# Kernel optimization log

Measured on AMD Instinct MI355X. Metric: run time of the kernel, lower is better.

## Reference

```python
import jax, jax.numpy as jnp
import numpy as np

P = 4096        # n_particles
D = 64          # embedding_dim
H = 4           # attention heads
HD = D // H     # head dim
N = 1_000_000   # n_collisions


def setup_inputs() -> dict:
    key = jax.random.key(0)
    ks = jax.random.split(key, 24)
    s = lambda k, shape, fan: jax.random.normal(k, shape, jnp.float32) / np.sqrt(fan)
    inp = {
        'times': jax.random.normal(ks[0], (N,), jnp.float32),
        'momentum_transfers': jax.random.normal(ks[1], (N,), jnp.float32),
        'positions': jax.random.normal(ks[2], (N,), jnp.float32),
        'particle_pairs': jax.random.randint(ks[3], (N, 2), 0, P),
        # event encoder: Linear(3, D)
        'W_enc': s(ks[4], (3, D), 3), 'b_enc': jnp.zeros((D,), jnp.float32),
        # learned particle embeddings
        'pemb': s(ks[5], (P, D), D),
        # MultiheadAttention projections (math layout: y = x @ W + b)
        'Wq': s(ks[6], (D, D), D), 'bq': jnp.zeros((D,), jnp.float32),
        'Wk': s(ks[7], (D, D), D), 'bk': jnp.zeros((D,), jnp.float32),
        'Wv': s(ks[8], (D, D), D), 'bv': jnp.zeros((D,), jnp.float32),
        'Wo': s(ks[9], (D, D), D), 'bo': jnp.zeros((D,), jnp.float32),
        # mass head: Linear(D, D//2) -> ReLU -> Linear(D//2, 1) -> Softplus
        'Wm1': s(ks[10], (D, D // 2), D), 'bm1': jnp.zeros((D // 2,), jnp.float32),
        'Wm2': s(ks[11], (D // 2, 1), D // 2), 'bm2': jnp.zeros((1,), jnp.float32),
        # diameter head
        'Wd1': s(ks[12], (D, D // 2), D), 'bd1': jnp.zeros((D // 2,), jnp.float32),
        'Wd2': s(ks[13], (D // 2, 1), D // 2), 'bd2': jnp.zeros((1,), jnp.float32),
    }
    return inp


def _forward(times, momentum_transfers, positions, particle_pairs,
             W_enc, b_enc, pemb, Wq, bq, Wk, bk, Wv, bv, Wo, bo,
             Wm1, bm1, Wm2, bm2, Wd1, bd1, Wd2, bd2):
    # 1. embed collision events: (N,3) -> (N,D), tanh
    feats = jnp.stack([times, momentum_transfers, positions], axis=-1)
    emb = jnp.tanh(feats @ W_enc + b_enc)  # (N, D)

    # 2. segment-mean pooling into particle bins (both endpoints of each pair)
    idx = particle_pairs.reshape(-1)                     # (2N,)
    vals = jnp.repeat(emb, 2, axis=0)                    # (2N, D) [p1,p2 per event]
    updates = jax.ops.segment_sum(vals, idx, num_segments=P)          # (P, D)
    counts = jax.ops.segment_sum(jnp.ones_like(idx, jnp.float32), idx,
                                 num_segments=P)                      # (P,)
    counts = jnp.clip(counts, 1.0)
    x = pemb + updates / counts[:, None]                 # (P, D)

    # 3. self-attention over particles (batch of 1)
    q = (x @ Wq + bq).reshape(P, H, HD)
    k = (x @ Wk + bk).reshape(P, H, HD)
    v = (x @ Wv + bv).reshape(P, H, HD)
    scale = 1.0 / np.sqrt(HD)
    scores = jnp.einsum('phd,qhd->hpq', q * scale, k)    # (H, P, P)
    attn = jax.nn.softmax(scores, axis=-1)
    ctx = jnp.einsum('hpq,qhd->phd', attn, v).reshape(P, D)
    x = ctx @ Wo + bo                                    # (P, D)

    # 4. prediction heads
    masses = jax.nn.softplus(
        (jax.nn.relu(x @ Wm1 + bm1) @ Wm2 + bm2)).squeeze(-1)  # (P,)
    diameters = jax.nn.softplus(
        (jax.nn.relu(x @ Wd1 + bd1) @ Wd2 + bd2)).squeeze(-1)  # (P,)
    return masses, diameters


def reference(times, momentum_transfers, positions, particle_pairs,
              W_enc, b_enc, pemb, Wq, bq, Wk, bk, Wv, bv, Wo, bo,
              Wm1, bm1, Wm2, bm2, Wd1, bd1, Wd2, bd2):
    return _forward(times, momentum_transfers, positions, particle_pairs,
                    W_enc, b_enc, pemb, Wq, bq, Wk, bk, Wv, bv, Wo, bo,
                    Wm1, bm1, Wm2, bm2, Wd1, bd1, Wd2, bd2)
```

## Files before the change

### kernel.cpp

```cpp
#include <hip/hip_runtime.h>
#include <hip/hip_fp16.h>
#include <math.h>

#define NP 1000000
#define NE (2 * NP)
#define P 4096
#define D 64
#define H 4
#define HD 16

#define NB 512
#define PBT 1024
#define SCB 128

#define KC 8

typedef short s4v __attribute__((ext_vector_type(4)));
typedef short s8v __attribute__((ext_vector_type(8)));
typedef float f4v __attribute__((ext_vector_type(4)));

__device__ __forceinline__ float softplus_f(float x) {
    return fmaxf(x, 0.0f) + log1pf(__expf(-fabsf(x)));
}
__device__ __forceinline__ unsigned short f2bf_rne(float f) {
    unsigned int b = __float_as_uint(f);
    b += 0x7fffu + ((b >> 16) & 1u);
    return (unsigned short)(b >> 16);
}

__global__ void __launch_bounds__(PBT) hist_pass(const int* __restrict__ pairs,
                                                 int* __restrict__ hists) {
    __shared__ int lh[P];
    const int tid = threadIdx.x, blk = blockIdx.x;
    for (int i = tid; i < P; i += PBT) lh[i] = 0;
    __syncthreads();
    const int lo = (int)(((long long)blk * NE) / NB);
    const int hi = (int)(((long long)(blk + 1) * NE) / NB);
    for (int i = lo + tid; i < hi; i += PBT) atomicAdd(&lh[pairs[i]], 1);
    __syncthreads();
    for (int i = tid; i < P; i += PBT) hists[(size_t)blk * P + i] = lh[i];
}

__global__ void __launch_bounds__(1024) scan_cols(int* __restrict__ hists,
                                                  int* __restrict__ totals) {
    __shared__ int buf[64][SCB];
    const int bo = blockIdx.x * SCB;
    const int t = threadIdx.x;
    const int col = t & (SCB - 1);
    const int row = t >> 7;
    int carry = 0;
    for (int c = 0; c < NB / 64; ++c) {
#pragma unroll
        for (int r8 = 0; r8 < 64; r8 += 8)
            buf[r8 + row][col] = hists[(size_t)(c * 64 + r8 + row) * P + bo + col];
        __syncthreads();
        if (t < SCB) {
            int cr = carry;
            for (int r = 0; r < 64; ++r) { int v = buf[r][t]; buf[r][t] = cr; cr += v; }
            carry = cr;
        }
        __syncthreads();
#pragma unroll
        for (int r8 = 0; r8 < 64; r8 += 8)
            hists[(size_t)(c * 64 + r8 + row) * P + bo + col] = buf[r8 + row][col];
        __syncthreads();
    }
    if (t < SCB) totals[bo + t] = carry;
}

__global__ void __launch_bounds__(1024) scan_bins(const int* __restrict__ totals,
                                                  int* __restrict__ bin_start) {
    __shared__ int sdat[1024];
    const int t = threadIdx.x;
    int a[4]; int s = 0;
#pragma unroll
    for (int k2 = 0; k2 < 4; ++k2) { a[k2] = totals[t * 4 + k2]; s += a[k2]; }
    sdat[t] = s;
    __syncthreads();
    for (int off = 1; off < 1024; off <<= 1) {
        int v = (t >= off) ? sdat[t - off] : 0;
        __syncthreads();
        sdat[t] += v;
        __syncthreads();
    }
    int run = sdat[t] - s;
#pragma unroll
    for (int k2 = 0; k2 < 4; ++k2) { bin_start[t * 4 + k2] = run; run += a[k2]; }
    if (t == 1023) bin_start[P] = run;
}

__global__ void __launch_bounds__(PBT) place_pass(
        const int* __restrict__ pairs, const float* __restrict__ times,
        const float* __restrict__ mom, const float* __restrict__ pos,
        const int* __restrict__ hists, const int* __restrict__ bin_start,
        uint2* __restrict__ sfeats) {
    __shared__ int lc[P];
    __shared__ int loff[P];
    const int tid = threadIdx.x, blk = blockIdx.x;
    for (int i = tid; i < P; i += PBT) {
        lc[i] = 0;
        loff[i] = bin_start[i] + hists[(size_t)blk * P + i];
    }
    __syncthreads();
    const int lo = (int)(((long long)blk * NE) / NB);
    const int hi = (int)(((long long)(blk + 1) * NE) / NB);
    int idx[4]; bool vld[4]; int bb[4]; uint2 ff[4];
#pragma unroll
    for (int j = 0; j < 4; ++j) {
        idx[j] = lo + tid + j * PBT;
        vld[j] = idx[j] < hi;
        int i2 = vld[j] ? idx[j] : lo;
        int ev = i2 >> 1;
        bb[j] = pairs[i2];
        __half2 tm = __floats2half2_rn(times[ev], mom[ev]);
        __half2 pz = __floats2half2_rn(pos[ev], 0.0f);
        ff[j].x = *(unsigned int*)&tm;
        ff[j].y = *(unsigned int*)&pz;
    }
    int rr[4];
#pragma unroll
    for (int j = 0; j < 4; ++j)
        rr[j] = vld[j] ? atomicAdd(&lc[bb[j]], 1) : 0;
#pragma unroll
    for (int j = 0; j < 4; ++j)
        if (vld[j]) sfeats[(size_t)loff[bb[j]] + rr[j]] = ff[j];
}

#define PDIM(w0_, w1_, w2_, b_, j)                                             \
    {                                                                          \
        float uA = fmaf(fAx, w0_, fmaf(fAy, w1_, fmaf(fAz, w2_, b_)));         \
        float uB = fmaf(fBx, w0_, fmaf(fBy, w1_, fmaf(fBz, w2_, b_)));         \
        float pA = __builtin_amdgcn_exp2f(uA) + 1.0f;                          \
        float pB = __builtin_amdgcn_exp2f(uB) + 1.0f;                          \
        racc[j] = fmaf(pA + pB, __builtin_amdgcn_rcpf(pA * pB), racc[j]);      \
    }
#define GBODY2()                                                               \
    PDIM(w0a[0], w1a[0], w2a[0], ba[0], 0)                                     \
    PDIM(w0a[1], w1a[1], w2a[1], ba[1], 1)                                     \
    PDIM(w0a[2], w1a[2], w2a[2], ba[2], 2)                                     \
    PDIM(w0a[3], w1a[3], w2a[3], ba[3], 3)                                     \
    PDIM(w0b[0], w1b[0], w2b[0], bbv[0], 4)                                    \
    PDIM(w0b[1], w1b[1], w2b[1], bbv[1], 5)                                    \
    PDIM(w0b[2], w1b[2], w2b[2], bbv[2], 6)                                    \
    PDIM(w0b[3], w1b[3], w2b[3], bbv[3], 7)

#define SDIM(w0_, w1_, w2_, b_, j)                                             \
    {                                                                          \
        float u = fmaf(fAx, w0_, fmaf(fAy, w1_, fmaf(fAz, w2_, b_)));          \
        racc[j] += __builtin_amdgcn_rcpf(__builtin_amdgcn_exp2f(u) + 1.0f);    \
    }
#define GBODY1()                                                               \
    SDIM(w0a[0], w1a[0], w2a[0], ba[0], 0)                                     \
    SDIM(w0a[1], w1a[1], w2a[1], ba[1], 1)                                     \
    SDIM(w0a[2], w1a[2], w2a[2], ba[2], 2)                                     \
    SDIM(w0a[3], w1a[3], w2a[3], ba[3], 3)                                     \
    SDIM(w0b[0], w1b[0], w2b[0], bbv[0], 4)                                    \
    SDIM(w0b[1], w1b[1], w2b[1], bbv[1], 5)                                    \
    SDIM(w0b[2], w1b[2], w2b[2], bbv[2], 6)                                    \
    SDIM(w0b[3], w1b[3], w2b[3], bbv[3], 7)

__global__ void __launch_bounds__(512) gather_kernel(
        const uint2* __restrict__ sfeats, const int* __restrict__ bin_start,
        const float* __restrict__ Wenc, const float* __restrict__ benc,
        const float* __restrict__ pemb, float* __restrict__ x) {
    __shared__ float sred[2][32][68];
    const int tid = threadIdx.x;
    const int wv = tid >> 6, ln = tid & 63;
    const int bi = wv >> 2, qh = wv & 3;
    const int es = ln & 7, dg = ln >> 3;
    const int b = blockIdx.x * 2 + bi;
    const int d0 = dg * 8;
    const float C = 2.8853900817779268f;
    f4v w0a = *(const f4v*)(Wenc + d0);          f4v w0b = *(const f4v*)(Wenc + d0 + 4);
    f4v w1a = *(const f4v*)(Wenc + D + d0);      f4v w1b = *(const f4v*)(Wenc + D + d0 + 4);
    f4v w2a = *(const f4v*)(Wenc + 2 * D + d0);  f4v w2b = *(const f4v*)(Wenc + 2 * D + d0 + 4);
    f4v ba  = *(const f4v*)(benc + d0);          f4v bbv = *(const f4v*)(benc + d0 + 4);
    w0a *= C; w0b *= C; w1a *= C; w1b *= C; w2a *= C; w2b *= C; ba *= C; bbv *= C;

    const int s0 = bin_start[b], s1 = bin_start[b + 1];
    const int cnt = s1 - s0;
    const int qs = (cnt + 3) >> 2;
    const int lo = s0 + qh * qs;
    const int hi = min(s0 + (qh + 1) * qs, s1);

    float racc[8];
#pragma unroll
    for (int j = 0; j < 8; ++j) racc[j] = 0.0f;
    int ncnt = 0;
    int base = lo;
    for (; base + 16 <= hi; base += 16) {
        uint2 uA = sfeats[base + es];
        uint2 uB = sfeats[base + 8 + es];
        float2 tA = __half22float2(*(__half2*)&uA.x);
        float fAx = tA.x, fAy = tA.y, fAz = __half2float(*(__half*)&uA.y);
        float2 tB = __half22float2(*(__half2*)&uB.x);
        float fBx = tB.x, fBy = tB.y, fBz = __half2float(*(__half*)&uB.y);
        GBODY2();
        ncnt += 2;
    }
    if (base + 8 <= hi) {
        uint2 uA = sfeats[base + es];
        float2 tA = __half22float2(*(__half2*)&uA.x);
        float fAx = tA.x, fAy = tA.y, fAz = __half2float(*(__half*)&uA.y);
        GBODY1();
        ncnt += 1;
        base += 8;
    }
    if (base < hi) {
        const int n = hi - base;
        const bool valid = es < n;
        uint2 uA = valid ? sfeats[base + es] : make_uint2(0u, 0u);
        float2 tA = __half22float2(*(__half2*)&uA.x);
        float fAx = tA.x, fAy = tA.y, fAz = __half2float(*(__half*)&uA.y);
        float save[8];
#pragma unroll
        for (int j = 0; j < 8; ++j) save[j] = racc[j];
        GBODY1();
        if (!valid) {
#pragma unroll
            for (int j = 0; j < 8; ++j) racc[j] = save[j];
        } else {
            ncnt += 1;
        }
    }
    const float fn = (float)ncnt;
    float* sw = &sred[bi][qh * 8 + es][d0];
#pragma unroll
    for (int j = 0; j < 8; ++j) sw[j] = fmaf(-2.0f, racc[j], fn);
    __syncthreads();
    if (tid < 128) {
        int bin = tid >> 6, dim = tid & 63;
        float s = 0.0f;
#pragma unroll
        for (int e2 = 0; e2 < 32; ++e2) s += sred[bin][e2][dim];
        int gb = blockIdx.x * 2 + bin;
        float c2 = (float)(bin_start[gb + 1] - bin_start[gb]);
        x[gb * D + dim] = pemb[gb * D + dim] + s / fmaxf(c2, 1.0f);
    }
}

__global__ void qkv_kernel(const float* __restrict__ x,
                           const float* __restrict__ Wq, const float* __restrict__ bq,
                           const float* __restrict__ Wk, const float* __restrict__ bk,
                           const float* __restrict__ Wv, const float* __restrict__ bv,
                           unsigned short* __restrict__ Qb, unsigned short* __restrict__ Kf,
                           unsigned short* __restrict__ Vf) {
    __shared__ float xs[4][D];
    const int r0 = blockIdx.x * 4;
    const int tid = threadIdx.x;
    xs[tid >> 6][tid & 63] = x[r0 * D + tid];
    __syncthreads();
    const int row = tid >> 6, col = tid & 63;
    float aq = bq[col], ak = bk[col], av = bv[col];
    for (int d = 0; d < D; ++d) {
        float xv = xs[row][d];
        aq = fmaf(xv, Wq[d * D + col], aq);
        ak = fmaf(xv, Wk[d * D + col], ak);
        av = fmaf(xv, Wv[d * D + col], av);
    }
    const int h = col >> 4, hd = col & 15, gr = r0 + row;
    Qb[((h * P + gr) << 4) + hd] = f2bf_rne(aq * 0.3606737602222409f);
    const int kb = gr >> 5, kk = gr & 31, up = kk >> 4;
    Kf[(((size_t)h * 128 + kb) * 64 + (hd >> 2) * 16 + (kk & 15)) * 8 + up * 4 + (hd & 3)] =
        f2bf_rne(ak);
    Vf[(((size_t)h * 128 + kb) * 64 + ((kk & 15) >> 2) * 16 + hd) * 8 + up * 4 + (kk & 3)] =
        f2bf_rne(av);
}

__global__ void __launch_bounds__(256) flash_kernel(
        const unsigned short* __restrict__ Qb, const unsigned short* __restrict__ Kf,
        const unsigned short* __restrict__ Vf,
        float* __restrict__ pl, float* __restrict__ pout) {
    const int bid = blockIdx.x;
    const int h  = bid & 3;
    const int qt = (bid >> 2) & 63;
    const int kc = bid >> 8;
    const int tid = threadIdx.x;
    const int wv = tid >> 6, lane = tid & 63;
    const int g = lane >> 4, li = lane & 15;
    const int q0 = qt * 64 + wv * 16;

    s8v qf = {0, 0, 0, 0, 0, 0, 0, 0};
    {
        s4v ql = *(const s4v*)(Qb + ((size_t)(h * P + q0 + li) << 4) + 4 * g);
        qf[0] = ql[0]; qf[1] = ql[1]; qf[2] = ql[2]; qf[3] = ql[3];
    }
    const unsigned short* Kh = Kf + (size_t)h * 128 * 512;
    const unsigned short* Vh = Vf + (size_t)h * 128 * 512;

    f4v accA = {0.f, 0.f, 0.f, 0.f};
    f4v accB = {0.f, 0.f, 0.f, 0.f};
    float lA = 0.f, lB = 0.f;
    const int kb0 = kc * (P / KC / 32);
    const int kb1 = kb0 + P / KC / 32;
#pragma unroll 4
    for (int kb = kb0; kb < kb1; kb += 2) {
        s8v kf1 = *(const s8v*)(Kh + ((size_t)kb * 64 + lane) * 8);
        s8v kf2 = *(const s8v*)(Kh + ((size_t)(kb + 1) * 64 + lane) * 8);
        s8v vf1 = *(const s8v*)(Vh + ((size_t)kb * 64 + lane) * 8);
        s8v vf2 = *(const s8v*)(Vh + ((size_t)(kb + 1) * 64 + lane) * 8);
        s8v ka1 = {kf1[0], kf1[1], kf1[2], kf1[3], 0, 0, 0, 0};
        s8v ka2 = {kf1[4], kf1[5], kf1[6], kf1[7], 0, 0, 0, 0};
        s8v ka3 = {kf2[0], kf2[1], kf2[2], kf2[3], 0, 0, 0, 0};
        s8v ka4 = {kf2[4], kf2[5], kf2[6], kf2[7], 0, 0, 0, 0};
        f4v z = {0.f, 0.f, 0.f, 0.f};
        f4v c1 = __builtin_amdgcn_mfma_f32_16x16x32_bf16(ka1, qf, z, 0, 0, 0);
        f4v c2 = __builtin_amdgcn_mfma_f32_16x16x32_bf16(ka2, qf, z, 0, 0, 0);
        f4v c3 = __builtin_amdgcn_mfma_f32_16x16x32_bf16(ka3, qf, z, 0, 0, 0);
        f4v c4 = __builtin_amdgcn_mfma_f32_16x16x32_bf16(ka4, qf, z, 0, 0, 0);
        float p0 = __builtin_amdgcn_exp2f(c1[0]), p1 = __builtin_amdgcn_exp2f(c1[1]);
        float p2 = __builtin_amdgcn_exp2f(c1[2]), p3 = __builtin_amdgcn_exp2f(c1[3]);
        float p4 = __builtin_amdgcn_exp2f(c2[0]), p5 = __builtin_amdgcn_exp2f(c2[1]);
        float p6 = __builtin_amdgcn_exp2f(c2[2]), p7 = __builtin_amdgcn_exp2f(c2[3]);
        float p8 = __builtin_amdgcn_exp2f(c3[0]), p9 = __builtin_amdgcn_exp2f(c3[1]);
        float pa = __builtin_amdgcn_exp2f(c3[2]), pb = __builtin_amdgcn_exp2f(c3[3]);
        float pc = __builtin_amdgcn_exp2f(c4[0]), pd = __builtin_amdgcn_exp2f(c4[1]);
        float pe = __builtin_amdgcn_exp2f(c4[2]), pf_ = __builtin_amdgcn_exp2f(c4[3]);
        lA += ((p0 + p1) + (p2 + p3)) + ((p4 + p5) + (p6 + p7));
        lB += ((p8 + p9) + (pa + pb)) + ((pc + pd) + (pe + pf_));
        s8v pf1, pf2;
        pf1[0] = (short)(__float_as_uint(p0) >> 16); pf1[1] = (short)(__float_as_uint(p1) >> 16);
        pf1[2] = (short)(__float_as_uint(p2) >> 16); pf1[3] = (short)(__float_as_uint(p3) >> 16);
        pf1[4] = (short)(__float_as_uint(p4) >> 16); pf1[5] = (short)(__float_as_uint(p5) >> 16);
        pf1[6] = (short)(__float_as_uint(p6) >> 16); pf1[7] = (short)(__float_as_uint(p7) >> 16);
        pf2[0] = (short)(__float_as_uint(p8) >> 16); pf2[1] = (short)(__float_as_uint(p9) >> 16);
        pf2[2] = (short)(__float_as_uint(pa) >> 16); pf2[3] = (short)(__float_as_uint(pb) >> 16);
        pf2[4] = (short)(__float_as_uint(pc) >> 16); pf2[5] = (short)(__float_as_uint(pd) >> 16);
        pf2[6] = (short)(__float_as_uint(pe) >> 16); pf2[7] = (short)(__float_as_uint(pf_) >> 16);
        accA = __builtin_amdgcn_mfma_f32_16x16x32_bf16(vf1, pf1, accA, 0, 0, 0);
        accB = __builtin_amdgcn_mfma_f32_16x16x32_bf16(vf2, pf2, accB, 0, 0, 0);
    }
    f4v acc = {accA[0] + accB[0], accA[1] + accB[1], accA[2] + accB[2], accA[3] + accB[3]};
    float l = lA + lB;
    l += __shfl_xor(l, 16, 64);
    l += __shfl_xor(l, 32, 64);
    const int q = q0 + li;
    const size_t gidx = (size_t)(h * P + q) * KC + kc;
    *(f4v*)(pout + gidx * 16 + 4 * g) = acc;
    if (lane < 16) pl[gidx] = l;
}

__global__ void heads_kernel(const float* __restrict__ pl, const float* __restrict__ pout,
                             const float* __restrict__ Wo, const float* __restrict__ bo,
                             const float* __restrict__ Wm1, const float* __restrict__ bm1,
                             const float* __restrict__ Wm2, const float* __restrict__ bm2,
                             const float* __restrict__ Wd1, const float* __restrict__ bd1,
                             const float* __restrict__ Wd2, const float* __restrict__ bd2,
                             float* __restrict__ out) {
    __shared__ float cs[4][D];
    __shared__ float x2[4][D];
    __shared__ float hid[4][D];
    const int r0 = blockIdx.x * 4;
    const int tid = threadIdx.x;
    const int row = tid >> 6, col = tid & 63;
    {
        const int h = col >> 4, hd = col & 15;
        const size_t gq = (size_t)(h * P + r0 + row);
        float L = 0.f, s = 0.f;
#pragma unroll
        for (int c = 0; c < KC; ++c) {
            L += pl[gq * KC + c];
            s += pout[(gq * KC + c) * 16 + hd];
        }
        cs[row][col] = s / L;
    }
    __syncthreads();
    float a = bo[col];
    for (int d = 0; d < D; ++d) a = fmaf(cs[row][d], Wo[d * D + col], a);
    x2[row][col] = a;
    __syncthreads();
    const int hc = col & 31;
    const float* W1 = (col < 32) ? Wm1 : Wd1;
    float hsum = (col < 32) ? bm1[hc] : bd1[hc];
    for (int d = 0; d < D; ++d) hsum = fmaf(x2[row][d], W1[d * 32 + hc], hsum);
    hsum = fmaxf(hsum, 0.0f);
    float w2 = (col < 32) ? Wm2[hc] : Wd2[hc];
    hid[row][col] = hsum * w2;
    __syncthreads();
    if (tid < 8) {
        int rr = tid >> 1, which = tid & 1;
        float s = which ? bd2[0] : bm2[0];
        for (int j2 = 0; j2 < 32; ++j2) s += hid[rr][which * 32 + j2];
        out[which * P + r0 + rr] = softplus_f(s);
    }
}

extern "C" void kernel_launch(void* const* d_in, const int* in_sizes, int n_in,
                              void* d_out, int out_size, void* d_ws, size_t ws_size,
                              hipStream_t stream) {
    const float* times = (const float*)d_in[0];
    const float* mom   = (const float*)d_in[1];
    const float* pos   = (const float*)d_in[2];
    const int*   pairs = (const int*)d_in[3];
    const float* Wenc  = (const float*)d_in[4];
    const float* benc  = (const float*)d_in[5];
    const float* pemb  = (const float*)d_in[6];
    const float* Wq = (const float*)d_in[7];   const float* bq = (const float*)d_in[8];
    const float* Wk = (const float*)d_in[9];   const float* bk = (const float*)d_in[10];
    const float* Wv = (const float*)d_in[11];  const float* bv = (const float*)d_in[12];
    const float* Wo = (const float*)d_in[13];  const float* bo = (const float*)d_in[14];
    const float* Wm1 = (const float*)d_in[15]; const float* bm1 = (const float*)d_in[16];
    const float* Wm2 = (const float*)d_in[17]; const float* bm2 = (const float*)d_in[18];
    const float* Wd1 = (const float*)d_in[19]; const float* bd1 = (const float*)d_in[20];
    const float* Wd2 = (const float*)d_in[21]; const float* bd2 = (const float*)d_in[22];

    char* wsb = (char*)d_ws;
    uint2* sfeats   = (uint2*)wsb;
    int* hists      = (int*)(wsb + (size_t)NE * 8);
    int* totals     = hists + (size_t)NB * P;
    int* bin_start  = totals + P;
    float* x        = (float*)(bin_start + P + 2);
    unsigned short* Qb = (unsigned short*)(x + P * D);
    unsigned short* Kf = Qb + (size_t)H * P * 16;
    unsigned short* Vf = Kf + (size_t)H * P * 16;
    float* pl       = (float*)(Vf + (size_t)H * P * 16);
    float* pout     = (float*)wsb;
    float* out      = (float*)d_out;

    hist_pass<<<NB, PBT, 0, stream>>>(pairs, hists);
    scan_cols<<<P / SCB, 1024, 0, stream>>>(hists, totals);
    scan_bins<<<1, 1024, 0, stream>>>(totals, bin_start);
    place_pass<<<NB, PBT, 0, stream>>>(pairs, times, mom, pos, hists, bin_start, sfeats);
    gather_kernel<<<P / 2, 512, 0, stream>>>(sfeats, bin_start, Wenc, benc, pemb, x);
    qkv_kernel<<<P / 4, 256, 0, stream>>>(x, Wq, bq, Wk, bk, Wv, bv, Qb, Kf, Vf);
    flash_kernel<<<H * (P / 64) * KC, 256, 0, stream>>>(Qb, Kf, Vf, pl, pout);
    heads_kernel<<<P / 4, 256, 0, stream>>>(pl, pout, Wo, bo, Wm1, bm1, Wm2, bm2,
                                            Wd1, bd1, Wd2, bd2, out);
}
```

Before: 127.7 us.

## Fuse bin scan into place pass and QKV projection into gather kernel

Removes the single-block scan_bins launch by having every place_pass block recompute the 4096-entry exclusive scan of totals redundantly, with block 0 writing bin_start for later kernels. Also removes the separate qkv_kernel and the x buffer round-trip by computing the Q/K/V projections inside gather_kernel from the pooled rows held in shared memory. This saves two kernel launches and a global write/read of x. In exchange, each place_pass block does an extra 1024-thread scan with about 20 barriers, and the gather kernel gains a tail phase where only 384 threads work.

```diff
diff --git a/kernel.cpp b/kernel.cpp
--- a/kernel.cpp
+++ b/kernel.cpp
@@ -68,39 +68,36 @@
     if (t < SCB) totals[bo + t] = carry;
 }
 
-__global__ void __launch_bounds__(1024) scan_bins(const int* __restrict__ totals,
-                                                  int* __restrict__ bin_start) {
-    __shared__ int sdat[1024];
-    const int t = threadIdx.x;
-    int a[4]; int s = 0;
-#pragma unroll
-    for (int k2 = 0; k2 < 4; ++k2) { a[k2] = totals[t * 4 + k2]; s += a[k2]; }
-    sdat[t] = s;
-    __syncthreads();
-    for (int off = 1; off < 1024; off <<= 1) {
-        int v = (t >= off) ? sdat[t - off] : 0;
-        __syncthreads();
-        sdat[t] += v;
-        __syncthreads();
-    }
-    int run = sdat[t] - s;
-#pragma unroll
-    for (int k2 = 0; k2 < 4; ++k2) { bin_start[t * 4 + k2] = run; run += a[k2]; }
-    if (t == 1023) bin_start[P] = run;
-}
-
 __global__ void __launch_bounds__(PBT) place_pass(
         const int* __restrict__ pairs, const float* __restrict__ times,
         const float* __restrict__ mom, const float* __restrict__ pos,
-        const int* __restrict__ hists, const int* __restrict__ bin_start,
-        uint2* __restrict__ sfeats) {
+        const int* __restrict__ hists, const int* __restrict__ totals,
+        int* __restrict__ bin_start, uint2* __restrict__ sfeats) {
     __shared__ int lc[P];
     __shared__ int loff[P];
+    __shared__ int sdat[1024];
     const int tid = threadIdx.x, blk = blockIdx.x;
-    for (int i = tid; i < P; i += PBT) {
+    int a[4]; int s = 0;
+#pragma unroll
+    for (int k2 = 0; k2 < 4; ++k2) { a[k2] = totals[tid * 4 + k2]; s += a[k2]; }
+    sdat[tid] = s;
+    __syncthreads();
+    for (int off = 1; off < 1024; off <<= 1) {
+        int v = (tid >= off) ? sdat[tid - off] : 0;
+        __syncthreads();
+        sdat[tid] += v;
+        __syncthreads();
+    }
+    int run = sdat[tid] - s;
+#pragma unroll
+    for (int k2 = 0; k2 < 4; ++k2) {
+        int i = tid * 4 + k2;
+        loff[i] = run + hists[(size_t)blk * P + i];
         lc[i] = 0;
-        loff[i] = bin_start[i] + hists[(size_t)blk * P + i];
-    }
+        if (blk == 0) bin_start[i] = run;
+        run += a[k2];
+    }
+    if (blk == 0 && tid == 1023) bin_start[P] = run;
     __syncthreads();
     const int lo = (int)(((long long)blk * NE) / NB);
     const int hi = (int)(((long long)(blk + 1) * NE) / NB);
@@ -162,8 +159,14 @@
 __global__ void __launch_bounds__(512) gather_kernel(
         const uint2* __restrict__ sfeats, const int* __restrict__ bin_start,
         const float* __restrict__ Wenc, const float* __restrict__ benc,
-        const float* __restrict__ pemb, float* __restrict__ x) {
+        const float* __restrict__ pemb,
+        const float* __restrict__ Wq, const float* __restrict__ bq,
+        const float* __restrict__ Wk, const float* __restrict__ bk,
+        const float* __restrict__ Wv, const float* __restrict__ bv,
+        unsigned short* __restrict__ Qb, unsigned short* __restrict__ Kf,
+        unsigned short* __restrict__ Vf) {
     __shared__ float sred[2][32][68];
+    __shared__ float xr[2][64];
     const int tid = threadIdx.x;
     const int wv = tid >> 6, ln = tid & 63;
     const int bi = wv >> 2, qh = wv & 3;
@@ -235,36 +238,32 @@
         for (int e2 = 0; e2 < 32; ++e2) s += sred[bin][e2][dim];
         int gb = blockIdx.x * 2 + bin;
         float c2 = (float)(bin_start[gb + 1] - bin_start[gb]);
-        x[gb * D + dim] = pemb[gb * D + dim] + s / fmaxf(c2, 1.0f);
-    }
-}
-
-__global__ void qkv_kernel(const float* __restrict__ x,
-                           const float* __restrict__ Wq, const float* __restrict__ bq,
-                           const float* __restrict__ Wk, const float* __restrict__ bk,
-                           const float* __restrict__ Wv, const float* __restrict__ bv,
-                           unsigned short* __restrict__ Qb, unsigned short* __restrict__ Kf,
-                           unsigned short* __restrict__ Vf) {
-    __shared__ float xs[4][D];
-    const int r0 = blockIdx.x * 4;
-    const int tid = threadIdx.x;
-    xs[tid >> 6][tid & 63] = x[r0 * D + tid];
-    __syncthreads();
-    const int row = tid >> 6, col = tid & 63;
-    float aq = bq[col], ak = bk[col], av = bv[col];
-    for (int d = 0; d < D; ++d) {
-        float xv = xs[row][d];
-        aq = fmaf(xv, Wq[d * D + col], aq);
-        ak = fmaf(xv, Wk[d * D + col], ak);
-        av = fmaf(xv, Wv[d * D + col], av);
-    }
-    const int h = col >> 4, hd = col & 15, gr = r0 + row;
-    Qb[((h * P + gr) << 4) + hd] = f2bf_rne(aq * 0.3606737602222409f);
-    const int kb = gr >> 5, kk = gr & 31, up = kk >> 4;
-    Kf[(((size_t)h * 128 + kb) * 64 + (hd >> 2) * 16 + (kk & 15)) * 8 + up * 4 + (hd & 3)] =
-        f2bf_rne(ak);
-    Vf[(((size_t)h * 128 + kb) * 64 + ((kk & 15) >> 2) * 16 + hd) * 8 + up * 4 + (kk & 3)] =
-        f2bf_rne(av);
+        xr[bin][dim] = pemb[gb * D + dim] + s / fmaxf(c2, 1.0f);
+    }
+    __syncthreads();
+    if (tid < 384) {
+        const int row = (tid >= 192) ? 1 : 0;
+        const int o = tid - row * 192;
+        const int which = o >> 6, col = o & 63;
+        const float* W = (which == 0) ? Wq : ((which == 1) ? Wk : Wv);
+        const float* bia = (which == 0) ? bq : ((which == 1) ? bk : bv);
+        float a = bia[col];
+#pragma unroll
+        for (int d = 0; d < D; ++d) a = fmaf(xr[row][d], W[d * D + col], a);
+        const int gr = blockIdx.x * 2 + row;
+        const int h = col >> 4, hd = col & 15;
+        if (which == 0) {
+            Qb[((h * P + gr) << 4) + hd] = f2bf_rne(a * 0.3606737602222409f);
+        } else {
+            const int kb = gr >> 5, kk = gr & 31, up = kk >> 4;
+            if (which == 1)
+                Kf[(((size_t)h * 128 + kb) * 64 + (hd >> 2) * 16 + (kk & 15)) * 8 +
+                   up * 4 + (hd & 3)] = f2bf_rne(a);
+            else
+                Vf[(((size_t)h * 128 + kb) * 64 + ((kk & 15) >> 2) * 16 + hd) * 8 +
+                   up * 4 + (kk & 3)] = f2bf_rne(a);
+        }
+    }
 }
 
 __global__ void __launch_bounds__(256) flash_kernel(
@@ -409,8 +408,7 @@
     int* hists      = (int*)(wsb + (size_t)NE * 8);
     int* totals     = hists + (size_t)NB * P;
     int* bin_start  = totals + P;
-    float* x        = (float*)(bin_start + P + 2);
-    unsigned short* Qb = (unsigned short*)(x + P * D);
+    unsigned short* Qb = (unsigned short*)(bin_start + P + 2);
     unsigned short* Kf = Qb + (size_t)H * P * 16;
     unsigned short* Vf = Kf + (size_t)H * P * 16;
     float* pl       = (float*)(Vf + (size_t)H * P * 16);
@@ -419,10 +417,10 @@
 
     hist_pass<<<NB, PBT, 0, stream>>>(pairs, hists);
     scan_cols<<<P / SCB, 1024, 0, stream>>>(hists, totals);
-    scan_bins<<<1, 1024, 0, stream>>>(totals, bin_start);
-    place_pass<<<NB, PBT, 0, stream>>>(pairs, times, mom, pos, hists, bin_start, sfeats);
-    gather_kernel<<<P / 2, 512, 0, stream>>>(sfeats, bin_start, Wenc, benc, pemb, x);
-    qkv_kernel<<<P / 4, 256, 0, stream>>>(x, Wq, bq, Wk, bk, Wv, bv, Qb, Kf, Vf);
+    place_pass<<<NB, PBT, 0, stream>>>(pairs, times, mom, pos, hists, totals,
+                                       bin_start, sfeats);
+    gather_kernel<<<P / 2, 512, 0, stream>>>(sfeats, bin_start, Wenc, benc, pemb,
+                                             Wq, bq, Wk, bk, Wv, bv, Qb, Kf, Vf);
     flash_kernel<<<H * (P / 64) * KC, 256, 0, stream>>>(Qb, Kf, Vf, pl, pout);
     heads_kernel<<<P / 4, 256, 0, stream>>>(pl, pout, Wo, bo, Wm1, bm1, Wm2, bm2,
                                             Wd1, bd1, Wd2, bd2, out);
```

New measurement: 123.5 us. -3.3%, faster.
